# Kernel tuning notes

Measured on AMD Instinct MI355X. Metric: run time of the kernel, lower is better.

## Reference

```python
import jax, jax.numpy as jnp
import numpy as np

N_NODES = 100000
N_EDGES = 3200000
NEG_SLOPE = 0.2  # PyG GATConv default leaky_relu slope


def gat_layer(x, src, dst, W, att_src, att_dst, bias, heads, out_ch, concat):
    N = x.shape[0]
    h = (x @ W).reshape(N, heads, out_ch)              # [N, H, C]
    a_src = jnp.sum(h * att_src[None], axis=-1)        # [N, H]
    a_dst = jnp.sum(h * att_dst[None], axis=-1)        # [N, H]
    e = jax.nn.leaky_relu(a_src[src] + a_dst[dst], NEG_SLOPE)  # [E, H]
    m = jax.ops.segment_max(e, dst, num_segments=N)    # segment softmax (stable)
    e = jnp.exp(e - m[dst])
    s = jax.ops.segment_sum(e, dst, num_segments=N)
    alpha = e / (s[dst] + 1e-16)                       # [E, H]
    msg = h[src] * alpha[:, :, None]                   # [E, H, C]
    out = jax.ops.segment_sum(msg, dst, num_segments=N)  # [N, H, C]
    out = out.reshape(N, heads * out_ch) if concat else out.mean(axis=1)
    return out + bias


def setup_inputs() -> dict:
    key = jax.random.key(0)
    ks = jax.random.split(key, 8)
    x = jax.random.normal(ks[0], (N_NODES, 512), dtype=jnp.float32)
    edge_index = jax.random.randint(ks[1], (2, N_EDGES), 0, N_NODES, dtype=jnp.int64)
    s1 = 1.0 / np.sqrt(512.0)
    s2 = 1.0 / np.sqrt(64.0)
    return {
        "x": x,
        "edge_index": edge_index,
        "W1": jax.random.normal(ks[2], (512, 64), dtype=jnp.float32) * s1,
        "att_src1": jax.random.normal(ks[3], (8, 8), dtype=jnp.float32) * s2,
        "att_dst1": jax.random.normal(ks[4], (8, 8), dtype=jnp.float32) * s2,
        "b1": jnp.zeros((64,), dtype=jnp.float32),
        "W2": jax.random.normal(ks[5], (64, 16), dtype=jnp.float32) * s2,
        "att_src2": jax.random.normal(ks[6], (1, 16), dtype=jnp.float32) * 0.25,
        "att_dst2": jax.random.normal(ks[7], (1, 16), dtype=jnp.float32) * 0.25,
        "b2": jnp.zeros((16,), dtype=jnp.float32),
    }


def reference(x, edge_index, W1, att_src1, att_dst1, b1, W2, att_src2, att_dst2, b2):
    N = x.shape[0]
    # add self-loops (PyG GATConv default) so every node has at least one edge
    loops = jnp.arange(N, dtype=edge_index.dtype)
    src = jnp.concatenate([edge_index[0], loops])
    dst = jnp.concatenate([edge_index[1], loops])
    # eval mode: dropout(p=0.6, training=False) is identity
    h = jax.nn.elu(gat_layer(x, src, dst, W1, att_src1, att_dst1, b1, 8, 8, True))
    z = gat_layer(h, src, dst, W2, att_src2, att_dst2, b2, 1, 16, False)
    return jax.nn.log_softmax(z, axis=1)
```

## Files before the change

kernel.cpp:

```cpp
#include <hip/hip_runtime.h>
#include <hip/hip_bf16.h>
#include <math.h>

#define LEAKY 0.2f
#define BSHIFT 7
#define NBUCK_MAX 1024
#define BCAP 6144
#define CHUNK 8192
#define CCAP 6656

typedef __attribute__((ext_vector_type(8))) short short8v;
typedef __attribute__((ext_vector_type(4))) float f32x4;

__device__ __forceinline__ unsigned pkbf(float a, float b) {
  __hip_bfloat162 t = __float22bfloat162_rn(make_float2(a, b));
  return *(unsigned*)&t;
}
__device__ __forceinline__ unsigned short f2bf(float f) {
  __hip_bfloat16 h = __float2bfloat16(f);
  return *(unsigned short*)&h;
}
__device__ __forceinline__ float bflo(unsigned u) { return __uint_as_float(u << 16); }
__device__ __forceinline__ float bfhi(unsigned u) { return __uint_as_float(u & 0xFFFF0000u); }

__global__ __launch_bounds__(256) void setup_kernel(
    const float* __restrict__ W1, unsigned short* __restrict__ w1t,
    int* __restrict__ bucketCursor) {
  int t = blockIdx.x * 256 + threadIdx.x;
  if (t < 64 * 512) {
    int k = t & 511, c = t >> 9;
    w1t[(size_t)c * 512 + k] = f2bf(W1[(size_t)k * 64 + c]);
  }
  if (t < NBUCK_MAX) bucketCursor[t] = t * BCAP;
}

__global__ __launch_bounds__(256) void binB_kernel(
    const int* __restrict__ src, const int* __restrict__ dst,
    int* __restrict__ bucketCursor, unsigned* __restrict__ ebuf,
    int E, int Etot, int NBUCK) {
  __shared__ unsigned stage[CHUNK];
  __shared__ unsigned short sbk[CHUNK];
  __shared__ int bcnt[NBUCK_MAX];
  __shared__ int bres[NBUCK_MAX];
  __shared__ int bcur[NBUCK_MAX];
  const int t = threadIdx.x;
  const int c0 = blockIdx.x * CHUNK;
  const int cnt = min(CHUNK, Etot - c0);
  for (int i = t; i < NBUCK_MAX; i += 256) bcnt[i] = 0;
  __syncthreads();
  for (int i = t; i < cnt; i += 256) {
    int g = c0 + i;
    int s, d;
    if (g < E) { s = src[g]; d = dst[g]; } else { s = d = g - E; }
    stage[i] = (unsigned)s | ((unsigned)(d & 127) << 20);
    sbk[i] = (unsigned short)(d >> BSHIFT);
    atomicAdd(&bcnt[d >> BSHIFT], 1);
  }
  __syncthreads();
  for (int i = t; i < NBUCK; i += 256) {
    int c = bcnt[i];
    bres[i] = c ? atomicAdd(&bucketCursor[i], c) : 0;
    bcur[i] = 0;
  }
  __syncthreads();
  for (int i = t; i < cnt; i += 256) {
    int b = sbk[i];
    int slot = bres[b] + atomicAdd(&bcur[b], 1);
    ebuf[slot] = stage[i];
  }
}

__global__ __launch_bounds__(256) void binC_kernel(
    const unsigned* __restrict__ ebuf, const int* __restrict__ bucketCursor,
    int2* __restrict__ seg, int* __restrict__ esrc, int N) {
  __shared__ unsigned stage[CCAP];
  __shared__ int hist[128];
  __shared__ int sA[128];
  __shared__ int curs[128];
  const int t = threadIdx.x;
  const int b = blockIdx.x;
  const int lo = b * BCAP;
  const int cnt = bucketCursor[b] - lo;
  const int base = b << BSHIFT;
  if (t < 128) hist[t] = 0;
  __syncthreads();
  for (int i = t; i < cnt; i += 256) {
    unsigned p = ebuf[lo + i];
    stage[i] = p;
    atomicAdd(&hist[p >> 20], 1);
  }
  __syncthreads();
  int v = 0;
  if (t < 128) { v = hist[t]; sA[t] = v; }
  __syncthreads();
  for (int off = 1; off < 128; off <<= 1) {
    int u = 0;
    if (t < 128 && t >= off) u = sA[t - off];
    __syncthreads();
    if (t < 128) sA[t] += u;
    __syncthreads();
  }
  if (t < 128) {
    int excl = sA[t] - v;
    curs[t] = excl;
    if (base + t < N) seg[base + t] = make_int2(lo + excl, v);
  }
  __syncthreads();
  for (int i = t; i < cnt; i += 256) {
    unsigned p = stage[i];
    int pos = atomicAdd(&curs[p >> 20], 1);
    esrc[lo + pos] = (int)(p & 0xFFFFFu);
  }
}

__global__ __launch_bounds__(256) void gemm1_kernel(
    const float* __restrict__ x, const unsigned short* __restrict__ w1t,
    unsigned short* __restrict__ h1b, int M) {
  __shared__ __align__(16) unsigned short AsU[128][40];
  __shared__ __align__(16) unsigned short BtU[64][40];
  const int tid = threadIdx.x;
  const int m0 = blockIdx.x * 128;
  const int w = tid >> 6, lane = tid & 63;
  const int l15 = lane & 15, lhi = lane >> 4;

  f32x4 acc[2][4];
#pragma unroll
  for (int r = 0; r < 2; ++r)
#pragma unroll
    for (int t = 0; t < 4; ++t) acc[r][t] = (f32x4){0.f, 0.f, 0.f, 0.f};

  for (int k0 = 0; k0 < 512; k0 += 32) {
#pragma unroll
    for (int u = 0; u < 4; ++u) {
      int q = u * 256 + tid;
      int r = q >> 3, c4 = q & 7;
      int gm = m0 + r;
      float4 v = make_float4(0.f, 0.f, 0.f, 0.f);
      if (gm < M) v = *(const float4*)(x + (size_t)gm * 512 + k0 + c4 * 4);
      *(uint2*)&AsU[r][c4 * 4] = make_uint2(pkbf(v.x, v.y), pkbf(v.z, v.w));
    }
    {
      int c = tid >> 2, kb = (tid & 3) * 8;
      short8v v = *(const short8v*)(w1t + (size_t)c * 512 + k0 + kb);
      *(short8v*)&BtU[c][kb] = v;
    }
    __syncthreads();

    short8v a0 = *(const short8v*)&AsU[32 * w + l15][lhi * 8];
    short8v a1 = *(const short8v*)&AsU[32 * w + 16 + l15][lhi * 8];
#pragma unroll
    for (int t = 0; t < 4; ++t) {
      short8v b = *(const short8v*)&BtU[16 * t + l15][lhi * 8];
      acc[0][t] = __builtin_amdgcn_mfma_f32_16x16x32_bf16(a0, b, acc[0][t], 0, 0, 0);
      acc[1][t] = __builtin_amdgcn_mfma_f32_16x16x32_bf16(a1, b, acc[1][t], 0, 0, 0);
    }
    __syncthreads();
  }
#pragma unroll
  for (int rt = 0; rt < 2; ++rt) {
#pragma unroll
    for (int t = 0; t < 4; ++t) {
#pragma unroll
      for (int reg = 0; reg < 4; ++reg) {
        int gm = m0 + 32 * w + 16 * rt + 4 * lhi + reg;
        if (gm < M) h1b[(size_t)gm * 64 + 16 * t + l15] = f2bf(acc[rt][t][reg]);
      }
    }
  }
}

__global__ __launch_bounds__(256) void agg1_kernel(
    const int2* __restrict__ seg, const int* __restrict__ esrc,
    const unsigned short* __restrict__ h1b, const float* __restrict__ att_src,
    const float* __restrict__ att_dst, const float* __restrict__ b1,
    unsigned short* __restrict__ hfeatb, int N) {
  int wid = (blockIdx.x * 256 + threadIdx.x) >> 6;
  int lane = threadIdx.x & 63;
  if (wid >= N) return;
  const int n = wid;
  const int eo = lane >> 3, q = lane & 7;
  float as[8], ad[8];
  {
    float4 t0 = *(const float4*)(att_src + 8 * q);
    float4 t1 = *(const float4*)(att_src + 8 * q + 4);
    as[0] = t0.x; as[1] = t0.y; as[2] = t0.z; as[3] = t0.w;
    as[4] = t1.x; as[5] = t1.y; as[6] = t1.z; as[7] = t1.w;
    t0 = *(const float4*)(att_dst + 8 * q);
    t1 = *(const float4*)(att_dst + 8 * q + 4);
    ad[0] = t0.x; ad[1] = t0.y; ad[2] = t0.z; ad[3] = t0.w;
    ad[4] = t1.x; ad[5] = t1.y; ad[6] = t1.z; ad[7] = t1.w;
  }
  float adn;
  {
    uint4 hv = *(const uint4*)(h1b + (size_t)n * 64 + 8 * q);
    adn = bflo(hv.x) * ad[0] + bfhi(hv.x) * ad[1] + bflo(hv.y) * ad[2] +
          bfhi(hv.y) * ad[3] + bflo(hv.z) * ad[4] + bfhi(hv.z) * ad[5] +
          bflo(hv.w) * ad[6] + bfhi(hv.w) * ad[7];
  }
  const int2 sg = seg[n];
  const int s0 = sg.x, s1 = sg.x + sg.y;
  float acc[8] = {0.f, 0.f, 0.f, 0.f, 0.f, 0.f, 0.f, 0.f};
  float psum = 0.f;
  for (int i = s0 + eo; i < s1; i += 8) {
    int s = esrc[i];
    uint4 hv = *(const uint4*)(h1b + (size_t)s * 64 + 8 * q);
    float g[8];
    g[0] = bflo(hv.x); g[1] = bfhi(hv.x); g[2] = bflo(hv.y); g[3] = bfhi(hv.y);
    g[4] = bflo(hv.z); g[5] = bfhi(hv.z); g[6] = bflo(hv.w); g[7] = bfhi(hv.w);
    float u = g[0] * as[0] + g[1] * as[1] + g[2] * as[2] + g[3] * as[3] +
              g[4] * as[4] + g[5] * as[5] + g[6] * as[6] + g[7] * as[7];
    float e = u + adn;
    e = e > 0.f ? e : LEAKY * e;
    float p = __expf(e);
#pragma unroll
    for (int j = 0; j < 8; ++j) acc[j] += p * g[j];
    psum += p;
  }
#pragma unroll
  for (int off = 8; off <= 32; off <<= 1) {
#pragma unroll
    for (int j = 0; j < 8; ++j) acc[j] += __shfl_xor(acc[j], off);
    psum += __shfl_xor(psum, off);
  }
  if (eo == 0) {
    float inv = 1.0f / (psum + 1e-16f);
    float4 b0 = *(const float4*)(b1 + 8 * q);
    float4 b14 = *(const float4*)(b1 + 8 * q + 4);
    float bb[8] = {b0.x, b0.y, b0.z, b0.w, b14.x, b14.y, b14.z, b14.w};
    float o[8];
#pragma unroll
    for (int j = 0; j < 8; ++j) {
      float v = acc[j] * inv + bb[j];
      o[j] = v > 0.f ? v : expm1f(v);
    }
    uint4 pk = make_uint4(pkbf(o[0], o[1]), pkbf(o[2], o[3]),
                          pkbf(o[4], o[5]), pkbf(o[6], o[7]));
    *(uint4*)(hfeatb + (size_t)n * 64 + 8 * q) = pk;
  }
}

__global__ __launch_bounds__(256) void gemm2_kernel(
    const unsigned short* __restrict__ hfeatb, const float* __restrict__ W2,
    unsigned short* __restrict__ g2b, int M) {
  __shared__ float Ws[1024];
  __shared__ float Hs[16][65];
  const int tid = threadIdx.x;
  const int n0 = blockIdx.x * 16;
  ((float4*)Ws)[tid] = ((const float4*)W2)[tid & 255];
  {
    uint2 v = *(const uint2*)(hfeatb + (size_t)n0 * 64 + tid * 4);
    int qq = tid * 4;
    int r = qq >> 6, c = qq & 63;
    Hs[r][c + 0] = bflo(v.x);
    Hs[r][c + 1] = bfhi(v.x);
    Hs[r][c + 2] = bflo(v.y);
    Hs[r][c + 3] = bfhi(v.y);
  }
  __syncthreads();
  const int nl = tid >> 4, c = tid & 15;
  float acc = 0.f;
#pragma unroll
  for (int k = 0; k < 64; ++k) acc += Hs[nl][k] * Ws[k * 16 + c];
  g2b[(size_t)(n0 + nl) * 16 + c] = f2bf(acc);
}

__global__ __launch_bounds__(256) void agg2_kernel(
    const int2* __restrict__ seg, const int* __restrict__ esrc,
    const unsigned short* __restrict__ g2b, const float* __restrict__ att_src,
    const float* __restrict__ att_dst, const float* __restrict__ b2,
    float* __restrict__ out, int N) {
  int wid = (blockIdx.x * 256 + threadIdx.x) >> 6;
  int lane = threadIdx.x & 63;
  if (wid >= N) return;
  const int n = wid;
  const int eo = lane >> 2, q = lane & 3;
  const float4 as4 = *(const float4*)(att_src + 4 * q);
  const float4 ad4 = *(const float4*)(att_dst + 4 * q);

  float adn;
  {
    uint2 gv = *(const uint2*)(g2b + (size_t)n * 16 + 4 * q);
    float un = bflo(gv.x) * ad4.x + bfhi(gv.x) * ad4.y +
               bflo(gv.y) * ad4.z + bfhi(gv.y) * ad4.w;
    un += __shfl_xor(un, 1);
    un += __shfl_xor(un, 2);
    adn = un;
  }

  const int2 sg = seg[n];
  const int s0 = sg.x, s1 = sg.x + sg.y;
  float a0 = 0.f, a1 = 0.f, a2 = 0.f, a3 = 0.f, psum = 0.f;
  for (int i = s0 + eo; i < s1; i += 16) {
    int s = esrc[i];
    uint2 gv = *(const uint2*)(g2b + (size_t)s * 16 + 4 * q);
    float g0 = bflo(gv.x), g1 = bfhi(gv.x), g2v = bflo(gv.y), g3 = bfhi(gv.y);
    float u = g0 * as4.x + g1 * as4.y + g2v * as4.z + g3 * as4.w;
    u += __shfl_xor(u, 1);
    u += __shfl_xor(u, 2);
    float e = u + adn;
    e = e > 0.f ? e : LEAKY * e;
    float p = __expf(e);
    a0 += p * g0; a1 += p * g1; a2 += p * g2v; a3 += p * g3;
    psum += p;
  }
#pragma unroll
  for (int off = 4; off <= 32; off <<= 1) {
    a0 += __shfl_xor(a0, off);
    a1 += __shfl_xor(a1, off);
    a2 += __shfl_xor(a2, off);
    a3 += __shfl_xor(a3, off);
    psum += __shfl_xor(psum, off);
  }

  float inv = 1.0f / (psum + 1e-16f);
  float z0 = a0 * inv + b2[4 * q + 0];
  float z1 = a1 * inv + b2[4 * q + 1];
  float z2 = a2 * inv + b2[4 * q + 2];
  float z3 = a3 * inv + b2[4 * q + 3];
  float mx = fmaxf(fmaxf(z0, z1), fmaxf(z2, z3));
  mx = fmaxf(mx, __shfl_xor(mx, 1));
  mx = fmaxf(mx, __shfl_xor(mx, 2));
  float ex = __expf(z0 - mx) + __expf(z1 - mx) + __expf(z2 - mx) + __expf(z3 - mx);
  ex += __shfl_xor(ex, 1);
  ex += __shfl_xor(ex, 2);
  float lse = mx + logf(ex);
  if (eo == 0)
    *(float4*)(out + (size_t)n * 16 + 4 * q) =
        make_float4(z0 - lse, z1 - lse, z2 - lse, z3 - lse);
}

extern "C" void kernel_launch(void* const* d_in, const int* in_sizes, int n_in,
                              void* d_out, int out_size, void* d_ws, size_t ws_size,
                              hipStream_t stream) {
  const float* x        = (const float*)d_in[0];
  const int*   ei       = (const int*)d_in[1];
  const float* W1       = (const float*)d_in[2];
  const float* att_src1 = (const float*)d_in[3];
  const float* att_dst1 = (const float*)d_in[4];
  const float* b1       = (const float*)d_in[5];
  const float* W2       = (const float*)d_in[6];
  const float* att_src2 = (const float*)d_in[7];
  const float* att_dst2 = (const float*)d_in[8];
  const float* b2       = (const float*)d_in[9];
  float* out = (float*)d_out;

  const int N = in_sizes[0] / 512;
  const int E = in_sizes[1] / 2;
  const int Etot = E + N;
  const int NBUCK = (N + 127) >> BSHIFT;

  char* base = (char*)d_ws;
  size_t off = 0;
  auto alloc = [&](size_t bytes) { void* p = base + off; off = (off + bytes + 15) & ~(size_t)15; return p; };
  unsigned short* h1b    = (unsigned short*)alloc((size_t)N * 64 * 2);
  unsigned short* hfeatb = (unsigned short*)alloc((size_t)N * 64 * 2);
  unsigned short* g2b    = (unsigned short*)alloc((size_t)N * 16 * 2);
  int*      esrc  = (int*)alloc((size_t)NBUCK * BCAP * 4);
  unsigned* ebuf  = (unsigned*)alloc((size_t)NBUCK * BCAP * 4);
  int2*     seg   = (int2*)alloc((size_t)N * 8);
  int* bucketCursor = (int*)alloc(NBUCK_MAX * 4);
  unsigned short* w1t = (unsigned short*)alloc(64 * 512 * 2);

  const int* srcI = ei;
  const int* dstI = ei + E;

  setup_kernel<<<128, 256, 0, stream>>>(W1, w1t, bucketCursor);
  binB_kernel<<<(Etot + CHUNK - 1) / CHUNK, 256, 0, stream>>>(
      srcI, dstI, bucketCursor, ebuf, E, Etot, NBUCK);
  binC_kernel<<<NBUCK, 256, 0, stream>>>(ebuf, bucketCursor, seg, esrc, N);

  gemm1_kernel<<<(N + 127) / 128, 256, 0, stream>>>(x, w1t, h1b, N);
  agg1_kernel<<<(N * 64 + 255) / 256, 256, 0, stream>>>(
      seg, esrc, h1b, att_src1, att_dst1, b1, hfeatb, N);

  gemm2_kernel<<<N / 16, 256, 0, stream>>>(hfeatb, W2, g2b, N);
  agg2_kernel<<<(N * 64 + 255) / 256, 256, 0, stream>>>(
      seg, esrc, g2b, att_src2, att_dst2, b2, out, N);
}
```

Baseline: 269.7 us.

## Fuse second-layer GEMM into agg1 and locally sort edges before scatter in binB

The layer-2 projection by W2 now runs inside the layer-1 aggregation kernel. Each wave multiplies its ELU output by W2 staged in shared memory and reduces across lanes with shuffles, so the hfeatb intermediate and the gemm2 launch go away. Separately, the binning kernel now does a block-local counting sort, with a histogram and an LDS prefix scan, before writing to the global bucket buffer, so stores to each bucket become contiguous. The cost is an extra pass over dst, more syncthreads and LDS use in binning, and every lane in agg1 now running the epilogue.

```diff
diff --git a/kernel.cpp b/kernel.cpp
--- a/kernel.cpp
+++ b/kernel.cpp
@@ -38,11 +38,13 @@
     const int* __restrict__ src, const int* __restrict__ dst,
     int* __restrict__ bucketCursor, unsigned* __restrict__ ebuf,
     int E, int Etot, int NBUCK) {
-  __shared__ unsigned stage[CHUNK];
-  __shared__ unsigned short sbk[CHUNK];
+  __shared__ unsigned sorted[CHUNK];
+  __shared__ unsigned short sbk2[CHUNK];
   __shared__ int bcnt[NBUCK_MAX];
-  __shared__ int bres[NBUCK_MAX];
+  __shared__ int bofs[NBUCK_MAX];
+  __shared__ int bdel[NBUCK_MAX];
   __shared__ int bcur[NBUCK_MAX];
+  __shared__ int wsum[256];
   const int t = threadIdx.x;
   const int c0 = blockIdx.x * CHUNK;
   const int cnt = min(CHUNK, Etot - c0);
@@ -50,23 +52,49 @@
   __syncthreads();
   for (int i = t; i < cnt; i += 256) {
     int g = c0 + i;
+    int d = (g < E) ? dst[g] : (g - E);
+    atomicAdd(&bcnt[d >> BSHIFT], 1);
+  }
+  __syncthreads();
+  {
+    int b4 = t * 4;
+    int e0 = bcnt[b4], e1 = bcnt[b4 + 1], e2 = bcnt[b4 + 2], e3 = bcnt[b4 + 3];
+    int s = e0 + e1 + e2 + e3;
+    wsum[t] = s;
+    __syncthreads();
+    for (int off = 1; off < 256; off <<= 1) {
+      int u = (t >= off) ? wsum[t - off] : 0;
+      __syncthreads();
+      wsum[t] += u;
+      __syncthreads();
+    }
+    int excl = wsum[t] - s;
+    bofs[b4] = excl;
+    bofs[b4 + 1] = excl + e0;
+    bofs[b4 + 2] = excl + e0 + e1;
+    bofs[b4 + 3] = excl + e0 + e1 + e2;
+  }
+  __syncthreads();
+  for (int i = t; i < NBUCK; i += 256) {
+    int c = bcnt[i];
+    int r = c ? atomicAdd(&bucketCursor[i], c) : 0;
+    bdel[i] = r - bofs[i];
+    bcur[i] = 0;
+  }
+  __syncthreads();
+  for (int i = t; i < cnt; i += 256) {
+    int g = c0 + i;
     int s, d;
     if (g < E) { s = src[g]; d = dst[g]; } else { s = d = g - E; }
-    stage[i] = (unsigned)s | ((unsigned)(d & 127) << 20);
-    sbk[i] = (unsigned short)(d >> BSHIFT);
-    atomicAdd(&bcnt[d >> BSHIFT], 1);
-  }
-  __syncthreads();
-  for (int i = t; i < NBUCK; i += 256) {
-    int c = bcnt[i];
-    bres[i] = c ? atomicAdd(&bucketCursor[i], c) : 0;
-    bcur[i] = 0;
-  }
-  __syncthreads();
-  for (int i = t; i < cnt; i += 256) {
-    int b = sbk[i];
-    int slot = bres[b] + atomicAdd(&bcur[b], 1);
-    ebuf[slot] = stage[i];
+    int b = d >> BSHIFT;
+    int pos = bofs[b] + atomicAdd(&bcur[b], 1);
+    sorted[pos] = (unsigned)s | ((unsigned)(d & 127) << 20);
+    sbk2[pos] = (unsigned short)b;
+  }
+  __syncthreads();
+  for (int i = t; i < cnt; i += 256) {
+    int b = sbk2[i];
+    ebuf[bdel[b] + i] = sorted[i];
   }
 }
 
@@ -173,7 +201,13 @@
     const int2* __restrict__ seg, const int* __restrict__ esrc,
     const unsigned short* __restrict__ h1b, const float* __restrict__ att_src,
     const float* __restrict__ att_dst, const float* __restrict__ b1,
-    unsigned short* __restrict__ hfeatb, int N) {
+    const float* __restrict__ W2, unsigned short* __restrict__ g2b, int N) {
+  __shared__ float Ws[1024];
+  {
+    float4 v = ((const float4*)W2)[threadIdx.x & 255];
+    *(float4*)&Ws[(threadIdx.x & 255) * 4] = v;
+  }
+  __syncthreads();
   int wid = (blockIdx.x * 256 + threadIdx.x) >> 6;
   int lane = threadIdx.x & 63;
   if (wid >= N) return;
@@ -222,46 +256,27 @@
     for (int j = 0; j < 8; ++j) acc[j] += __shfl_xor(acc[j], off);
     psum += __shfl_xor(psum, off);
   }
-  if (eo == 0) {
-    float inv = 1.0f / (psum + 1e-16f);
-    float4 b0 = *(const float4*)(b1 + 8 * q);
-    float4 b14 = *(const float4*)(b1 + 8 * q + 4);
-    float bb[8] = {b0.x, b0.y, b0.z, b0.w, b14.x, b14.y, b14.z, b14.w};
-    float o[8];
-#pragma unroll
-    for (int j = 0; j < 8; ++j) {
-      float v = acc[j] * inv + bb[j];
-      o[j] = v > 0.f ? v : expm1f(v);
-    }
-    uint4 pk = make_uint4(pkbf(o[0], o[1]), pkbf(o[2], o[3]),
-                          pkbf(o[4], o[5]), pkbf(o[6], o[7]));
-    *(uint4*)(hfeatb + (size_t)n * 64 + 8 * q) = pk;
-  }
-}
-
-__global__ __launch_bounds__(256) void gemm2_kernel(
-    const unsigned short* __restrict__ hfeatb, const float* __restrict__ W2,
-    unsigned short* __restrict__ g2b, int M) {
-  __shared__ float Ws[1024];
-  __shared__ float Hs[16][65];
-  const int tid = threadIdx.x;
-  const int n0 = blockIdx.x * 16;
-  ((float4*)Ws)[tid] = ((const float4*)W2)[tid & 255];
-  {
-    uint2 v = *(const uint2*)(hfeatb + (size_t)n0 * 64 + tid * 4);
-    int qq = tid * 4;
-    int r = qq >> 6, c = qq & 63;
-    Hs[r][c + 0] = bflo(v.x);
-    Hs[r][c + 1] = bfhi(v.x);
-    Hs[r][c + 2] = bflo(v.y);
-    Hs[r][c + 3] = bfhi(v.y);
-  }
-  __syncthreads();
-  const int nl = tid >> 4, c = tid & 15;
-  float acc = 0.f;
-#pragma unroll
-  for (int k = 0; k < 64; ++k) acc += Hs[nl][k] * Ws[k * 16 + c];
-  g2b[(size_t)(n0 + nl) * 16 + c] = f2bf(acc);
+  float inv = 1.0f / (psum + 1e-16f);
+  float4 b0 = *(const float4*)(b1 + 8 * q);
+  float4 b14 = *(const float4*)(b1 + 8 * q + 4);
+  float bb[8] = {b0.x, b0.y, b0.z, b0.w, b14.x, b14.y, b14.z, b14.w};
+  float o[8];
+#pragma unroll
+  for (int j = 0; j < 8; ++j) {
+    float v = acc[j] * inv + bb[j];
+    o[j] = v > 0.f ? v : expm1f(v);
+  }
+  float p0 = 0.f, p1 = 0.f;
+#pragma unroll
+  for (int j = 0; j < 8; ++j) {
+    float2 wv = *(const float2*)&Ws[(8 * q + j) * 16 + 2 * eo];
+    p0 += o[j] * wv.x;
+    p1 += o[j] * wv.y;
+  }
+  p0 += __shfl_xor(p0, 1); p0 += __shfl_xor(p0, 2); p0 += __shfl_xor(p0, 4);
+  p1 += __shfl_xor(p1, 1); p1 += __shfl_xor(p1, 2); p1 += __shfl_xor(p1, 4);
+  if (q == 0)
+    *(unsigned*)&g2b[(size_t)n * 16 + 2 * eo] = pkbf(p0, p1);
 }
 
 __global__ __launch_bounds__(256) void agg2_kernel(
@@ -352,9 +367,8 @@
   char* base = (char*)d_ws;
   size_t off = 0;
   auto alloc = [&](size_t bytes) { void* p = base + off; off = (off + bytes + 15) & ~(size_t)15; return p; };
-  unsigned short* h1b    = (unsigned short*)alloc((size_t)N * 64 * 2);
-  unsigned short* hfeatb = (unsigned short*)alloc((size_t)N * 64 * 2);
-  unsigned short* g2b    = (unsigned short*)alloc((size_t)N * 16 * 2);
+  unsigned short* h1b = (unsigned short*)alloc((size_t)N * 64 * 2);
+  unsigned short* g2b = (unsigned short*)alloc((size_t)N * 16 * 2);
   int*      esrc  = (int*)alloc((size_t)NBUCK * BCAP * 4);
   unsigned* ebuf  = (unsigned*)alloc((size_t)NBUCK * BCAP * 4);
   int2*     seg   = (int2*)alloc((size_t)N * 8);
@@ -371,9 +385,8 @@
 
   gemm1_kernel<<<(N + 127) / 128, 256, 0, stream>>>(x, w1t, h1b, N);
   agg1_kernel<<<(N * 64 + 255) / 256, 256, 0, stream>>>(
-      seg, esrc, h1b, att_src1, att_dst1, b1, hfeatb, N);
-
-  gemm2_kernel<<<N / 16, 256, 0, stream>>>(hfeatb, W2, g2b, N);
+      seg, esrc, h1b, att_src1, att_dst1, b1, W2, g2b, N);
+
   agg2_kernel<<<(N * 64 + 255) / 256, 256, 0, stream>>>(
       seg, esrc, g2b, att_src2, att_dst2, b2, out, N);
 }
```

Measured after the change: 277.6 us. +2.9%, slower.
